# Performance work log

Measured on AMD Instinct MI355X. Metric: run time of the kernel, lower is better.

The kernel has to match this reference:

```python
import jax, jax.numpy as jnp
import numpy as np

B, S, HID = 2, 2048, 2048
H, D = 16, 128  # heads, head_dim == kernel_hidden_size
GATE_NORM = 16.0
CLAMP_MIN = -50.0


def gla(q, k, v, gk):
    # fused_recurrent_gla: S_t = diag(exp(gk_t)) S_{t-1} + k_t^T v_t; o_t = (q_t*scale) @ S_t
    # q,k,v,gk: [B,H,S,D]
    scale = D ** -0.5
    qs = jnp.moveaxis(q, 2, 0) * scale  # [S,B,H,D]
    ks = jnp.moveaxis(k, 2, 0)
    vs = jnp.moveaxis(v, 2, 0)
    gs = jnp.moveaxis(gk, 2, 0)

    def step(state, xs):
        q_t, k_t, v_t, g_t = xs  # each [B,H,D]
        state = state * jnp.exp(g_t)[..., None] + k_t[..., None] * v_t[..., None, :]
        o_t = jnp.einsum('bhk,bhkv->bhv', q_t, state)
        return state, o_t

    init = jnp.zeros((q.shape[0], H, D, D), q.dtype)
    _, out = jax.lax.scan(step, init, (qs, ks, vs, gs))
    return jnp.moveaxis(out, 0, 2)  # [B,H,S,D]


def setup_inputs() -> dict:
    key = jax.random.key(0)
    ks = jax.random.split(key, 8)
    std = 0.02
    hidden_states = jax.random.normal(ks[0], (B, S, HID), jnp.float32)
    Wq = jax.random.normal(ks[1], (HID, HID), jnp.float32) * std
    Wk = jax.random.normal(ks[2], (HID, HID), jnp.float32) * std
    Wv = jax.random.normal(ks[3], (HID, HID), jnp.float32) * std
    Wo = jax.random.normal(ks[4], (HID, HID), jnp.float32) * std
    Wg1 = jnp.eye(HID, dtype=jnp.float32)  # nn.init.eye_
    bg1 = jnp.zeros((HID,), jnp.float32)
    Wg2 = jnp.eye(HID, dtype=jnp.float32)
    bg2 = jnp.zeros((HID,), jnp.float32)
    alpha_list = jax.random.uniform(ks[5], (2,), jnp.float32)
    return dict(hidden_states=hidden_states, Wq=Wq, Wk=Wk, Wv=Wv, Wo=Wo,
                Wg1=Wg1, bg1=bg1, Wg2=Wg2, bg2=bg2, alpha_list=alpha_list)


def reference(hidden_states, Wq, Wk, Wv, Wo, Wg1, bg1, Wg2, bg2, alpha_list):
    b, s, _ = hidden_states.shape

    def split_heads(x):  # [b,s,hid] -> [b,h,s,d]
        return x.reshape(b, s, H, D).transpose(0, 2, 1, 3)

    q = split_heads(hidden_states @ Wq.T)
    k = split_heads(hidden_states @ Wk.T)
    v = split_heads(hidden_states @ Wv.T)

    def gate(Wg, bg):
        g = split_heads(hidden_states @ Wg.T + bg)
        g = jax.nn.log_sigmoid(g) / GATE_NORM
        return jnp.maximum(g, CLAMP_MIN)

    gk = gate(Wg1, bg1)
    gk2 = gate(Wg2, bg2)

    o1 = gla(q, k, v, gk)
    o2 = gla(q, k, v, gk2)

    a = jax.nn.softmax(alpha_list)
    attn = a[0] * o1 + a[1] * o2  # [b,h,s,d]
    attn = attn.transpose(0, 2, 1, 3).reshape(b, s, HID)
    return attn @ Wo.T
```

## Files before the change

### kernel.cpp

```cpp
#include <hip/hip_runtime.h>
#include <cstdint>
#include <cstddef>


#define BB     2
#define SEQ    2048
#define HIDN   2048
#define NH     16
#define DD     128
#define CHUNK  64
#define NCHUNK (SEQ / CHUNK)
#define NBH    (BB * NH)
#define NELC   8388608
#define WELC   4194304
static constexpr float QSCALE = 0.08838834764831845f;

typedef __bf16 bf16_t;
typedef _Float16 half_t;
typedef short  short8 __attribute__((ext_vector_type(8)));
typedef float  f32x4  __attribute__((ext_vector_type(4)));

__device__ __forceinline__ float bf2f(short u) {
  return (float)__builtin_bit_cast(bf16_t, u);
}
__device__ __forceinline__ short f2bf(float f) {
  return __builtin_bit_cast(short, (bf16_t)f);
}
__device__ __forceinline__ float hf2f(short u) {
  return (float)__builtin_bit_cast(half_t, u);
}
__device__ __forceinline__ short f2hf(float f) {
  return __builtin_bit_cast(short, (half_t)f);
}

__device__ __forceinline__ void gload_lds16(const void* g, void* l) {
  __builtin_amdgcn_global_load_lds(
      (__attribute__((address_space(1))) unsigned int*)g,
      (__attribute__((address_space(3))) unsigned int*)l, 16, 0, 0);
}

#define VMW2 asm volatile("s_waitcnt vmcnt(2)" ::: "memory")
#define VMW0 asm volatile("s_waitcnt vmcnt(0)" ::: "memory")
#define SBAR __builtin_amdgcn_s_barrier()


#define STG_A(buf, kt, h)                                                   \
  {                                                                         \
    const size_t ko = (size_t)(kt) * 64;                                    \
    gload_lds16(Ag + (size_t)((h) * 128) * HIDN + ko,                       \
                (void*)&As[buf][((h) * 128 + wave * 8) * 64]);              \
    gload_lds16(Ag + (size_t)((h) * 128 + 64) * HIDN + ko,                  \
                (void*)&As[buf][((h) * 128 + 64 + wave * 8) * 64]);         \
  }

#define STG_B(buf, kt, h)                                                   \
  {                                                                         \
    const size_t ko = (size_t)(kt) * 64;                                    \
    gload_lds16(Bg + (size_t)((h) * 128) * HIDN + ko,                       \
                (void*)&Bs[buf][((h) * 128 + wave * 8) * 64]);              \
    gload_lds16(Bg + (size_t)((h) * 128 + 64) * HIDN + ko,                  \
                (void*)&Bs[buf][((h) * 128 + 64 + wave * 8) * 64]);         \
  }

#define LDA(mh, rb)                                                         \
  {                                                                         \
    _Pragma("unroll") for (int f = 0; f < 4; f++) {                         \
      const int row = wm * 128 + (mh) * 64 + f * 16 + l16;                  \
      af[f][0] = *(const short8*)&As[rb][row * 64 + ((qd ^ ro) << 3)];      \
      af[f][1] =                                                            \
          *(const short8*)&As[rb][row * 64 + (((4 + qd) ^ ro) << 3)];       \
    }                                                                       \
  }

#define LDB2(j0, rb)                                                        \
  {                                                                         \
    _Pragma("unroll") for (int g = 0; g < 2; g++) {                         \
      const int col = wn * 64 + ((j0) + g) * 16 + l16;                      \
      bfr[(j0) + g][0] =                                                    \
          *(const short8*)&Bs[rb][col * 64 + ((qd ^ ro) << 3)];             \
      bfr[(j0) + g][1] =                                                    \
          *(const short8*)&Bs[rb][col * 64 + (((4 + qd) ^ ro) << 3)];       \
    }                                                                       \
  }

#define MQ(mh, nh)                                                          \
  {                                                                         \
    __builtin_amdgcn_s_setprio(1);                                          \
    _Pragma("unroll") for (int ks = 0; ks < 2; ks++)                        \
    _Pragma("unroll") for (int f = 0; f < 4; f++)                           \
    _Pragma("unroll") for (int g = 0; g < 2; g++)                           \
      acc[(mh) * 4 + f][(nh) * 2 + g] =                                     \
          __builtin_amdgcn_mfma_f32_16x16x32_bf16(                          \
              af[f][ks], bfr[(nh) * 2 + g][ks],                             \
              acc[(mh) * 4 + f][(nh) * 2 + g], 0, 0, 0);                    \
    __builtin_amdgcn_s_setprio(0);                                          \
  }

__device__ __forceinline__ void gemm256(const bf16_t* __restrict__ A,
                                        const bf16_t* __restrict__ Bw,
                                        const float*  __restrict__ bias,
                                        bf16_t* __restrict__ outb,
                                        float*  __restrict__ outf, int epi) {
  __shared__ short As[2][256 * 64];
  __shared__ short Bs[2][256 * 64];
  const int tm   = blockIdx.x * 256;
  const int tn   = blockIdx.y * 256;
  const int tid  = threadIdx.x;
  const int wave = tid >> 6;
  const int lane = tid & 63;
  const int wm   = wave >> 2;
  const int wn   = wave & 3;
  const int qd   = lane >> 4;
  const int l16  = lane & 15;
  const int ro   = l16 & 7;
  const int gc   = (lane & 7) ^ (lane >> 3);

  const short* Ag =
      (const short*)A + (size_t)(tm + wave * 8 + (lane >> 3)) * HIDN + gc * 8;
  const short* Bg =
      (const short*)Bw + (size_t)(tn + wave * 8 + (lane >> 3)) * HIDN + gc * 8;

  f32x4 acc[8][4];
#pragma unroll
  for (int i = 0; i < 8; i++)
#pragma unroll
    for (int j = 0; j < 4; j++) acc[i][j] = (f32x4){0.f, 0.f, 0.f, 0.f};
  short8 af[4][2], bfr[4][2];

  STG_A(0, 0, 0); STG_A(0, 0, 1); STG_B(0, 0, 0); STG_B(0, 0, 1);
  STG_A(1, 1, 0);
  VMW2;
  SBAR;

  for (int t = 0; t < 16; t++) {
    LDA(0, 0); LDB2(0, 0);
    STG_A(1, 2 * t + 1, 1);
    SBAR; MQ(0, 0); SBAR;
    LDB2(2, 0);
    STG_B(1, 2 * t + 1, 0);
    SBAR; MQ(0, 1); SBAR;
    LDA(1, 0);
    STG_B(1, 2 * t + 1, 1);
    SBAR; MQ(1, 1); SBAR;
    if (t < 15) { STG_A(0, 2 * t + 2, 0); }
    SBAR; MQ(1, 0);
    if (t < 15) { VMW2; } else { VMW0; }
    SBAR;
    LDA(0, 1); LDB2(0, 1);
    if (t < 15) { STG_A(0, 2 * t + 2, 1); }
    SBAR; MQ(0, 0); SBAR;
    LDB2(2, 1);
    if (t < 15) { STG_B(0, 2 * t + 2, 0); }
    SBAR; MQ(0, 1); SBAR;
    LDA(1, 1);
    if (t < 15) { STG_B(0, 2 * t + 2, 1); }
    SBAR; MQ(1, 1); SBAR;
    if (t < 15) { STG_A(1, 2 * t + 3, 0); }
    SBAR; MQ(1, 0);
    if (t < 15) { VMW2; }
    SBAR;
  }

#pragma unroll
  for (int i = 0; i < 8; i++)
#pragma unroll
    for (int j = 0; j < 4; j++)
#pragma unroll
      for (int r = 0; r < 4; r++) {
        const int row =
            tm + wm * 128 + (i >> 2) * 64 + (i & 3) * 16 + qd * 4 + r;
        const int col = tn + wn * 64 + j * 16 + l16;
        float v = acc[i][j][r];
        if (epi == 1) {
          v += bias[col];
          const float ls = fminf(v, 0.f) - log1pf(__expf(-fabsf(v)));
          v = fmaxf(ls * 0.0625f, -50.f);
        }
        if (epi == 2) outf[(size_t)row * HIDN + col] = v;
        else          outb[(size_t)row * HIDN + col] = (bf16_t)v;
      }
}

__global__ __launch_bounds__(512, 2) void k_gemm_proj(
    const bf16_t* __restrict__ Xb,
    const bf16_t* __restrict__ W0, const bf16_t* __restrict__ W1,
    const bf16_t* __restrict__ W2, const bf16_t* __restrict__ W3,
    const bf16_t* __restrict__ W4,
    const float* __restrict__ bg1, const float* __restrict__ bg2,
    bf16_t* __restrict__ Qb, bf16_t* __restrict__ Kb, bf16_t* __restrict__ Vb,
    bf16_t* __restrict__ G1b, bf16_t* __restrict__ G2b) {
  const int z = blockIdx.z;
  const bf16_t* Ws[5] = {W0, W1, W2, W3, W4};
  bf16_t* Os[5] = {Qb, Kb, Vb, G1b, G2b};
  const float* bias = (z == 3) ? bg1 : ((z == 4) ? bg2 : nullptr);
  gemm256(Xb, Ws[z], bias, Os[z], nullptr, (z >= 3) ? 1 : 0);
}

__global__ __launch_bounds__(512, 2) void k_gemm_out(
    const bf16_t* __restrict__ attnB, const bf16_t* __restrict__ Wob,
    float* __restrict__ out) {
  gemm256(attnB, Wob, nullptr, nullptr, out, 2);
}

__global__ __launch_bounds__(256) void k_cvt_all(
    const float* __restrict__ hid, const float* __restrict__ wq,
    const float* __restrict__ wk, const float* __restrict__ wv,
    const float* __restrict__ wg1, const float* __restrict__ wg2,
    const float* __restrict__ wo, bf16_t* __restrict__ Xb,
    bf16_t* __restrict__ Wd, bf16_t* __restrict__ Wcur,
    bf16_t* __restrict__ WoB) {
  const int y = blockIdx.y;
  const float* srcs[7] = {hid, wq, wk, wv, wg1, wg2, wo};
  bf16_t* dsts[7] = {Xb, Wd, Wd + WELC, Wd + 2 * WELC, Wd + 3 * WELC, Wcur,
                     WoB};
  const int n = (y == 0) ? NELC : WELC;
  const float* src = srcs[y];
  bf16_t* dst = dsts[y];
  const int idx = (blockIdx.x * 256 + threadIdx.x) * 4;
  if (idx < n) {
    const float4 f = *(const float4*)(src + idx);
    dst[idx + 0] = (bf16_t)f.x; dst[idx + 1] = (bf16_t)f.y;
    dst[idx + 2] = (bf16_t)f.z; dst[idx + 3] = (bf16_t)f.w;
  }
}

__global__ __launch_bounds__(256) void k_zero(float* __restrict__ out) {
  out[(size_t)blockIdx.x * 256 + threadIdx.x] = 0.f;
}

__global__ __launch_bounds__(64) void k_gc(bf16_t* __restrict__ G1b,
                                           bf16_t* __restrict__ G2b,
                                           float* __restrict__ Btot) {
  const int n = blockIdx.x, b = blockIdx.y >> 2, slab = blockIdx.y & 3;
  const int e = blockIdx.z;
  short* P = (short*)(e ? G2b : G1b);
  const int d0 = slab * 512 + threadIdx.x * 8;
  const size_t base = ((size_t)(b * SEQ + n * CHUNK)) * HIDN + d0;
  float c[8] = {0.f, 0.f, 0.f, 0.f, 0.f, 0.f, 0.f, 0.f};
  for (int t = 0; t < CHUNK; t++) {
    short* p = P + base + (size_t)t * HIDN;
    const short8 g = *(const short8*)p;
    short8 o;
#pragma unroll
    for (int j = 0; j < 8; j++) { c[j] += bf2f(g[j]); o[j] = f2hf(c[j]); }
    *(short8*)p = o;
  }
  const int bh = b * 16 + (d0 >> 7);
  float* bp = Btot + ((size_t)(e * NBH + bh) * NCHUNK + n) * DD + (d0 & 127);
#pragma unroll
  for (int j = 0; j < 8; j++) bp[j] = c[j];
}

template <int ACC>
__global__ __launch_bounds__(256) void k_sA(
    const bf16_t* __restrict__ Qb, const bf16_t* __restrict__ Kb,
    const bf16_t* __restrict__ Vb, const bf16_t* __restrict__ Gc,
    bf16_t* __restrict__ UT, const float* __restrict__ alpha,
    bf16_t* __restrict__ attn) {
  const int n = blockIdx.x, bh = blockIdx.y;
  const int b = bh >> 4, h = bh & 15;
  const size_t rbase = ((size_t)(b * SEQ + n * CHUNK)) * HIDN + h * DD;
  const int tid = threadIdx.x;
  const int wave = tid >> 6, lane = tid & 63, qd = lane >> 4, l16 = lane & 15;
  __shared__ short vT[128 * 66];
  __shared__ short k2s[64 * 128];
  __shared__ short r3[128 * 66];
  __shared__ short Ps[64 * 72];
  const float mx = fmaxf(alpha[0], alpha[1]);
  const float x0 = __expf(alpha[0] - mx), x1 = __expf(alpha[1] - mx);
  const float wsc = ((ACC ? x1 : x0) / (x0 + x1)) * QSCALE;

  const short* Kp = (const short*)Kb;
  const short* Vp = (const short*)Vb;
  const short* Gp = (const short*)Gc;
  const short* Qp = (const short*)Qb;

#pragma unroll
  for (int rep = 0; rep < 4; rep++) {
    const int slot = rep * 256 + tid;
    const int t = slot >> 4, ch = slot & 15;
    const size_t ga = rbase + (size_t)t * HIDN + ch * 8;
    const short8 vv = *(const short8*)(Vp + ga);
    const short8 kk = *(const short8*)(Kp + ga);
    const short8 cc = *(const short8*)(Gp + ga);
    const short8 c6 = *(const short8*)(Gp + rbase + (size_t)63 * HIDN + ch * 8);
    short8 k2v;
#pragma unroll
    for (int j = 0; j < 8; j++) {
      const int d = ch * 8 + j;
      vT[d * 66 + t] = vv[j];
      const float c = hf2f(cc[j]);
      const float kf = bf2f(kk[j]);
      k2v[j] = f2bf(kf * __expf(-c));
      r3[d * 66 + t] = f2bf(kf * __expf(hf2f(c6[j]) - c));
    }
    *(short8*)&k2s[t * 128 + ((ch ^ (t & 7)) << 3)] = k2v;
  }
  __syncthreads();

  {
    const int m0 = (wave >> 1) * 64, n0 = (wave & 1) * 64;
    const int* vTi = (const int*)vT;
    const int* r3i = (const int*)r3;
    f32x4 uacc[4][4];
#pragma unroll
    for (int i = 0; i < 4; i++)
#pragma unroll
      for (int j = 0; j < 4; j++) uacc[i][j] = (f32x4){0.f, 0.f, 0.f, 0.f};
#pragma unroll
    for (int ks = 0; ks < 2; ks++) {
      const int ch = ks * 4 + qd;
      short8 af[4], bfv[4];
#pragma unroll
      for (int i = 0; i < 4; i++) {
        const int dv = m0 + i * 16 + l16;
        const int ba = dv * 33 + ch * 4;
#pragma unroll
        for (int w2 = 0; w2 < 4; w2++) {
          const int v = vTi[ba + w2];
          af[i][2 * w2] = (short)(v & 0xffff);
          af[i][2 * w2 + 1] = (short)((unsigned)v >> 16);
        }
      }
#pragma unroll
      for (int j = 0; j < 4; j++) {
        const int dk = n0 + j * 16 + l16;
        const int ba = dk * 33 + ch * 4;
#pragma unroll
        for (int w2 = 0; w2 < 4; w2++) {
          const int v = r3i[ba + w2];
          bfv[j][2 * w2] = (short)(v & 0xffff);
          bfv[j][2 * w2 + 1] = (short)((unsigned)v >> 16);
        }
      }
#pragma unroll
      for (int i = 0; i < 4; i++)
#pragma unroll
        for (int j = 0; j < 4; j++)
          uacc[i][j] = __builtin_amdgcn_mfma_f32_16x16x32_bf16(
              af[i], bfv[j], uacc[i][j], 0, 0, 0);
    }
    short* Uo = (short*)UT + (size_t)(bh * NCHUNK + n) * (DD * DD);
#pragma unroll
    for (int i = 0; i < 4; i++)
#pragma unroll
      for (int j = 0; j < 4; j++)
#pragma unroll
        for (int r = 0; r < 4; r++) {
          const int dv = m0 + i * 16 + qd * 4 + r;
          const int dk = n0 + j * 16 + l16;
          Uo[dv * 128 + (((dk >> 3) ^ (dv & 7)) << 3) + (dk & 7)] =
              f2bf(uacc[i][j][r]);
        }
  }
  __syncthreads();

#pragma unroll
  for (int rep = 0; rep < 4; rep++) {
    const int slot = rep * 256 + tid;
    const int t = slot >> 4, ch = slot & 15;
    const size_t ga = rbase + (size_t)t * HIDN + ch * 8;
    const short8 qq = *(const short8*)(Qp + ga);
    const short8 cc = *(const short8*)(Gp + ga);
    short8 o;
#pragma unroll
    for (int j = 0; j < 8; j++)
      o[j] = f2bf(bf2f(qq[j]) * wsc * __expf(hf2f(cc[j])));
    *(short8*)&r3[t * 128 + ((ch ^ (t & 7)) << 3)] = o;
  }
  __syncthreads();

  {
    f32x4 pacc[4];
#pragma unroll
    for (int j = 0; j < 4; j++) pacc[j] = (f32x4){0.f, 0.f, 0.f, 0.f};
    const int tq = wave * 16 + l16;
#pragma unroll
    for (int ks = 0; ks < 4; ks++) {
      const int ch = ks * 4 + qd;
      const short8 a = *(const short8*)&r3[tq * 128 + ((ch ^ (tq & 7)) << 3)];
#pragma unroll
      for (int j = 0; j < 4; j++) {
        const int s = j * 16 + l16;
        const short8 bq =
            *(const short8*)&k2s[s * 128 + ((ch ^ (s & 7)) << 3)];
        pacc[j] =
            __builtin_amdgcn_mfma_f32_16x16x32_bf16(a, bq, pacc[j], 0, 0, 0);
      }
    }
#pragma unroll
    for (int j = 0; j < 4; j++)
#pragma unroll
      for (int r = 0; r < 4; r++) {
        const int t = wave * 16 + qd * 4 + r, s = j * 16 + l16;
        Ps[t * 72 + s] = (t >= s) ? f2bf(pacc[j][r]) : (short)0;
      }
  }
  __syncthreads();

  f32x4 oacc[8];
#pragma unroll
  for (int j = 0; j < 8; j++) oacc[j] = (f32x4){0.f, 0.f, 0.f, 0.f};
  {
    const int* vTi = (const int*)vT;
    const int tq = wave * 16 + l16;
#pragma unroll
    for (int ks = 0; ks < 2; ks++) {
      const int ch = ks * 4 + qd;
      const short8 a = *(const short8*)&Ps[tq * 72 + ch * 8];
#pragma unroll
      for (int j = 0; j < 8; j++) {
        const int dv = j * 16 + l16;
        const int ba = dv * 33 + ch * 4;
        short8 bq;
#pragma unroll
        for (int w2 = 0; w2 < 4; w2++) {
          const int v = vTi[ba + w2];
          bq[2 * w2] = (short)(v & 0xffff);
          bq[2 * w2 + 1] = (short)((unsigned)v >> 16);
        }
        oacc[j] =
            __builtin_amdgcn_mfma_f32_16x16x32_bf16(a, bq, oacc[j], 0, 0, 0);
      }
    }
  }
#pragma unroll
  for (int j = 0; j < 8; j++)
#pragma unroll
    for (int r = 0; r < 4; r++) {
      const int t = wave * 16 + qd * 4 + r;
      const int dv = j * 16 + l16;
      bf16_t* p = &attn[rbase + (size_t)t * HIDN + dv];
      if (ACC) *p = (bf16_t)((float)*p + oacc[j][r]);
      else     *p = (bf16_t)oacc[j][r];
    }
}

__global__ __launch_bounds__(256) void k_s2(bf16_t* __restrict__ UT,
                                            const float* __restrict__ Btot) {
  const int dg = blockIdx.x, bh = blockIdx.y;
  const int dv = dg * 8 + (threadIdx.x >> 5);
  const int dk0 = (threadIdx.x & 31) * 4;
  const int pos = dv * 128 + (((dk0 >> 3) ^ (dv & 7)) << 3) + (dk0 & 7);
  float st[4] = {0.f, 0.f, 0.f, 0.f};
  for (int nn = 0; nn < NCHUNK; nn++) {
    short* p = (short*)UT + (size_t)(bh * NCHUNK + nn) * (DD * DD) + pos;
    const float4 bp =
        *(const float4*)(Btot + (size_t)(bh * NCHUNK + nn) * DD + dk0);
    short u0 = p[0], u1 = p[1], u2 = p[2], u3 = p[3];
    p[0] = f2bf(st[0]); p[1] = f2bf(st[1]);
    p[2] = f2bf(st[2]); p[3] = f2bf(st[3]);
    st[0] = st[0] * __expf(bp.x) + bf2f(u0);
    st[1] = st[1] * __expf(bp.y) + bf2f(u1);
    st[2] = st[2] * __expf(bp.z) + bf2f(u2);
    st[3] = st[3] * __expf(bp.w) + bf2f(u3);
  }
}

__global__ __launch_bounds__(256) void k_s3b(
    const bf16_t* __restrict__ Qb, const bf16_t* __restrict__ Gc,
    const bf16_t* __restrict__ UT, const float* __restrict__ alpha,
    const int e, bf16_t* __restrict__ attn) {
  const int n = blockIdx.x, bh = blockIdx.y;
  const int b = bh >> 4, h = bh & 15;
  const size_t rbase = ((size_t)(b * SEQ + n * CHUNK)) * HIDN + h * DD;
  const int tid = threadIdx.x;
  const int wave = tid >> 6, lane = tid & 63, qd = lane >> 4, l16 = lane & 15;
  __shared__ short qh[64 * 128];
  __shared__ short Ss[128 * 128];
  const float mx = fmaxf(alpha[0], alpha[1]);
  const float x0 = __expf(alpha[0] - mx), x1 = __expf(alpha[1] - mx);
  const float wsc = ((e ? x1 : x0) / (x0 + x1)) * QSCALE;

  const short* Sp = (const short*)UT + (size_t)(bh * NCHUNK + n) * (DD * DD);
#pragma unroll
  for (int rep = 0; rep < 8; rep++) {
    const int c = rep * 256 + tid;
    gload_lds16(Sp + c * 8, &Ss[c * 8]);
  }
  const short* Qp = (const short*)Qb;
  const short* Gp = (const short*)Gc;
#pragma unroll
  for (int rep = 0; rep < 4; rep++) {
    const int slot = rep * 256 + tid;
    const int t = slot >> 4, ch = slot & 15;
    const size_t ga = rbase + (size_t)t * HIDN + ch * 8;
    const short8 qq = *(const short8*)(Qp + ga);
    const short8 cc = *(const short8*)(Gp + ga);
    short8 o;
#pragma unroll
    for (int j = 0; j < 8; j++)
      o[j] = f2bf(bf2f(qq[j]) * wsc * __expf(hf2f(cc[j])));
    *(short8*)&qh[t * 128 + ((ch ^ (t & 7)) << 3)] = o;
  }
  __syncthreads();

  f32x4 oacc[8];
#pragma unroll
  for (int j = 0; j < 8; j++) oacc[j] = (f32x4){0.f, 0.f, 0.f, 0.f};
  const int tq = wave * 16 + l16;
#pragma unroll
  for (int ks = 0; ks < 4; ks++) {
    const int ch = ks * 4 + qd;
    const short8 a = *(const short8*)&qh[tq * 128 + ((ch ^ (tq & 7)) << 3)];
#pragma unroll
    for (int j = 0; j < 8; j++) {
      const int dv = j * 16 + l16;
      const short8 bq = *(const short8*)&Ss[dv * 128 + ((ch ^ (dv & 7)) << 3)];
      oacc[j] =
          __builtin_amdgcn_mfma_f32_16x16x32_bf16(a, bq, oacc[j], 0, 0, 0);
    }
  }
#pragma unroll
  for (int j = 0; j < 8; j++)
#pragma unroll
    for (int r = 0; r < 4; r++) {
      const int t = wave * 16 + qd * 4 + r;
      const int dv = j * 16 + l16;
      bf16_t* p = &attn[rbase + (size_t)t * HIDN + dv];
      *p = (bf16_t)((float)*p + oacc[j][r]);
    }
}

extern "C" void kernel_launch(void* const* d_in, const int* in_sizes, int n_in,
                              void* d_out, int out_size, void* d_ws,
                              size_t ws_size, hipStream_t stream) {
  const float* hid  = (const float*)d_in[0];
  const float* wq   = (const float*)d_in[1];
  const float* wk   = (const float*)d_in[2];
  const float* wv   = (const float*)d_in[3];
  const float* wo   = (const float*)d_in[4];
  const float* wg1  = (const float*)d_in[5];
  const float* bg1  = (const float*)d_in[6];
  const float* wg2  = (const float*)d_in[7];
  const float* bg2  = (const float*)d_in[8];
  const float* alph = (const float*)d_in[9];
  float* out = (float*)d_out;
  (void)in_sizes; (void)n_in; (void)out_size;

  char* ws = (char*)d_ws;
  size_t off = 0;
  auto alloc = [&](size_t bytes) -> void* {
    void* p = ws + off;
    off += (bytes + 255) & ~(size_t)255;
    return p;
  };
  const size_t NEL = NELC, WEL = WELC;
  bf16_t* Xb   = (bf16_t*)alloc(NEL * 2);
  bf16_t* Wcur = (bf16_t*)alloc(WEL * 2);
  bf16_t* WoB  = (bf16_t*)alloc(WEL * 2);
  bf16_t* Qb   = (bf16_t*)alloc(NEL * 2);
  bf16_t* Kb   = (bf16_t*)alloc(NEL * 2);
  bf16_t* Vb   = (bf16_t*)alloc(NEL * 2);
  bf16_t* G1b  = (bf16_t*)alloc(NEL * 2);
  bf16_t* G2b  = (bf16_t*)alloc(NEL * 2);
  float*  Btot = (float*) alloc((size_t)2 * NBH * NCHUNK * DD * 4);
  bf16_t* Wd = (bf16_t*)d_out;
  bf16_t* UT = (bf16_t*)d_out;

  if (off > ws_size) {
    k_zero<<<dim3((unsigned)(NEL / 256)), 256, 0, stream>>>(out);
    return;
  }

  k_cvt_all<<<dim3(8192, 7), 256, 0, stream>>>(hid, wq, wk, wv, wg1, wg2, wo,
                                               Xb, Wd, Wcur, WoB);
  k_gemm_proj<<<dim3(16, 8, 5), 512, 0, stream>>>(
      Xb, Wd, Wd + WEL, Wd + 2 * WEL, Wd + 3 * WEL, Wcur, bg1, bg2, Qb, Kb, Vb,
      G1b, G2b);
  k_gc<<<dim3(NCHUNK, BB * 4, 2), 64, 0, stream>>>(G1b, G2b, Btot);

  const dim3 gs(NCHUNK, NBH), g2(16, NBH);
  const size_t BSTRIDE = (size_t)NBH * NCHUNK * DD;
  k_sA<0><<<gs, 256, 0, stream>>>(Qb, Kb, Vb, G1b, UT, alph, Xb);
  k_s2<<<g2, 256, 0, stream>>>(UT, Btot);
  k_s3b<<<gs, 256, 0, stream>>>(Qb, G1b, UT, alph, 0, Xb);
  k_sA<1><<<gs, 256, 0, stream>>>(Qb, Kb, Vb, G2b, UT, alph, Xb);
  k_s2<<<g2, 256, 0, stream>>>(UT, Btot + BSTRIDE);
  k_s3b<<<gs, 256, 0, stream>>>(Qb, G2b, UT, alph, 1, Xb);

  k_gemm_out<<<dim3(16, 8), 512, 0, stream>>>(Xb, WoB, out);
}
```

Baseline: 591.4 us.

## Restructure GEMM main loop into simple double-buffered pipeline with fewer barriers

Rewrites the GEMM k-loop as a 32-iteration ping-pong over two LDS buffers. It also reorganizes the A/B staging partitions so each prefetch quarter lands in exactly the rows the next MFMA phase reads. Most of the paired barriers around each MFMA block are removed in favour of vmcnt-based waits, with only about three barriers per k-step. This aims to cut barrier stalls and let global-to-LDS loads overlap compute. The risk is that the wait counts and barrier placement no longer cover every read-after-write or write-after-read hazard on the LDS buffers, which could produce races.

```diff
diff --git a/kernel.cpp b/kernel.cpp
--- a/kernel.cpp
+++ b/kernel.cpp
@@ -39,27 +39,29 @@
       (__attribute__((address_space(3))) unsigned int*)l, 16, 0, 0);
 }
 
-#define VMW2 asm volatile("s_waitcnt vmcnt(2)" ::: "memory")
-#define VMW0 asm volatile("s_waitcnt vmcnt(0)" ::: "memory")
+#define WVM4 asm volatile("s_waitcnt vmcnt(4)" ::: "memory")
+#define WVM2 asm volatile("s_waitcnt vmcnt(2)" ::: "memory")
+#define WVM0 asm volatile("s_waitcnt vmcnt(0)" ::: "memory")
 #define SBAR __builtin_amdgcn_s_barrier()
 
 
-#define STG_A(buf, kt, h)                                                   \
+#define STG_A(buf, kt, p)                                                   \
   {                                                                         \
     const size_t ko = (size_t)(kt) * 64;                                    \
-    gload_lds16(Ag + (size_t)((h) * 128) * HIDN + ko,                       \
-                (void*)&As[buf][((h) * 128 + wave * 8) * 64]);              \
-    gload_lds16(Ag + (size_t)((h) * 128 + 64) * HIDN + ko,                  \
-                (void*)&As[buf][((h) * 128 + 64 + wave * 8) * 64]);         \
-  }
-
-#define STG_B(buf, kt, h)                                                   \
+    gload_lds16(Ag + (size_t)((p) * 64) * HIDN + ko,                        \
+                (void*)&As[buf][((p) * 64 + wave * 8) * 64]);               \
+    gload_lds16(Ag + (size_t)((p) * 64 + 128) * HIDN + ko,                  \
+                (void*)&As[buf][((p) * 64 + 128 + wave * 8) * 64]);         \
+  }
+
+#define STG_B(buf, kt, p)                                                   \
   {                                                                         \
+    const int cb0 = (wave >> 2) * 64 + (p) * 32 + (wave & 3) * 8;           \
     const size_t ko = (size_t)(kt) * 64;                                    \
-    gload_lds16(Bg + (size_t)((h) * 128) * HIDN + ko,                       \
-                (void*)&Bs[buf][((h) * 128 + wave * 8) * 64]);              \
-    gload_lds16(Bg + (size_t)((h) * 128 + 64) * HIDN + ko,                  \
-                (void*)&Bs[buf][((h) * 128 + 64 + wave * 8) * 64]);         \
+    gload_lds16(Bg + (size_t)cb0 * HIDN + ko,                               \
+                (void*)&Bs[buf][cb0 * 64]);                                 \
+    gload_lds16(Bg + (size_t)(cb0 + 128) * HIDN + ko,                       \
+                (void*)&Bs[buf][(cb0 + 128) * 64]);                         \
   }
 
 #define LDA(mh, rb)                                                         \
@@ -118,7 +120,7 @@
   const short* Ag =
       (const short*)A + (size_t)(tm + wave * 8 + (lane >> 3)) * HIDN + gc * 8;
   const short* Bg =
-      (const short*)Bw + (size_t)(tn + wave * 8 + (lane >> 3)) * HIDN + gc * 8;
+      (const short*)Bw + (size_t)(tn + (lane >> 3)) * HIDN + gc * 8;
 
   f32x4 acc[8][4];
 #pragma unroll
@@ -127,38 +129,32 @@
     for (int j = 0; j < 4; j++) acc[i][j] = (f32x4){0.f, 0.f, 0.f, 0.f};
   short8 af[4][2], bfr[4][2];
 
-  STG_A(0, 0, 0); STG_A(0, 0, 1); STG_B(0, 0, 0); STG_B(0, 0, 1);
-  STG_A(1, 1, 0);
-  VMW2;
+  STG_A(0, 0, 0); STG_B(0, 0, 0); STG_B(0, 0, 1); STG_A(0, 0, 1);
+  WVM0;
   SBAR;
 
-  for (int t = 0; t < 16; t++) {
-    LDA(0, 0); LDB2(0, 0);
-    STG_A(1, 2 * t + 1, 1);
-    SBAR; MQ(0, 0); SBAR;
-    LDB2(2, 0);
-    STG_B(1, 2 * t + 1, 0);
-    SBAR; MQ(0, 1); SBAR;
-    LDA(1, 0);
-    STG_B(1, 2 * t + 1, 1);
-    SBAR; MQ(1, 1); SBAR;
-    if (t < 15) { STG_A(0, 2 * t + 2, 0); }
-    SBAR; MQ(1, 0);
-    if (t < 15) { VMW2; } else { VMW0; }
+  for (int t = 0; t < 32; t++) {
+    const int cur = t & 1, nx = cur ^ 1;
+    LDA(0, cur);
+    LDB2(0, cur);
+    if (t < 31) { STG_A(nx, t + 1, 0); }
+    MQ(0, 0);
+    if (t < 31) { WVM4; } else { WVM2; }
     SBAR;
-    LDA(0, 1); LDB2(0, 1);
-    if (t < 15) { STG_A(0, 2 * t + 2, 1); }
-    SBAR; MQ(0, 0); SBAR;
-    LDB2(2, 1);
-    if (t < 15) { STG_B(0, 2 * t + 2, 0); }
-    SBAR; MQ(0, 1); SBAR;
-    LDA(1, 1);
-    if (t < 15) { STG_B(0, 2 * t + 2, 1); }
-    SBAR; MQ(1, 1); SBAR;
-    if (t < 15) { STG_A(1, 2 * t + 3, 0); }
-    SBAR; MQ(1, 0);
-    if (t < 15) { VMW2; }
+    LDB2(2, cur);
+    if (t < 31) { STG_B(nx, t + 1, 0); }
+    MQ(0, 1);
+    if (t < 31) { WVM4; } else { WVM0; }
     SBAR;
+    LDA(1, cur);
+    if (t < 31) { STG_B(nx, t + 1, 1); }
+    MQ(1, 1);
+    if (t < 31) { STG_A(nx, t + 1, 1); }
+    MQ(1, 0);
+    if (t < 31) {
+      WVM4;
+      SBAR;
+    }
   }
 
 #pragma unroll
```

Result: slower. 605.9 us (+2.4%).

## Reorder GEMM LDS staging halves and use explicit ds_read with manual waits

Applied to the files above, without the earlier changes.

Changes which rows each staging half loads so that A halves match the mh split and B halves match each wave-column's nh split. This lets the pipeline drop two barriers per iteration. LDS fragment reads become inline-asm ds_read_b128 followed by an explicit lgkmcnt(0) wait and a sched barrier before each MFMA block, giving manual control over instruction scheduling. The risk is a race if the new half-to-row mapping does not exactly match the consumption order once barriers are removed.

```diff
diff --git a/kernel.cpp b/kernel.cpp
--- a/kernel.cpp
+++ b/kernel.cpp
@@ -39,36 +39,50 @@
       (__attribute__((address_space(3))) unsigned int*)l, 16, 0, 0);
 }
 
+__device__ __forceinline__ short8 ldsr128(const short* p) {
+  short8 r;
+  asm volatile("ds_read_b128 %0, %1"
+               : "=v"(r)
+               : "v"((unsigned)(unsigned long long)
+                         (__attribute__((address_space(3))) const short*)p));
+  return r;
+}
+
 #define VMW2 asm volatile("s_waitcnt vmcnt(2)" ::: "memory")
 #define VMW0 asm volatile("s_waitcnt vmcnt(0)" ::: "memory")
+#define WAIT_LDS                                          \
+  do {                                                    \
+    asm volatile("s_waitcnt lgkmcnt(0)" ::: "memory");    \
+    __builtin_amdgcn_sched_barrier(0);                    \
+  } while (0)
 #define SBAR __builtin_amdgcn_s_barrier()
 
 
 #define STG_A(buf, kt, h)                                                   \
   {                                                                         \
     const size_t ko = (size_t)(kt) * 64;                                    \
-    gload_lds16(Ag + (size_t)((h) * 128) * HIDN + ko,                       \
-                (void*)&As[buf][((h) * 128 + wave * 8) * 64]);              \
-    gload_lds16(Ag + (size_t)((h) * 128 + 64) * HIDN + ko,                  \
-                (void*)&As[buf][((h) * 128 + 64 + wave * 8) * 64]);         \
+    gload_lds16(Ag + (size_t)((h) * 64) * HIDN + ko,                        \
+                (void*)&As[buf][((h) * 64 + wave * 8) * 64]);               \
+    gload_lds16(Ag + (size_t)((h) * 64 + 128) * HIDN + ko,                  \
+                (void*)&As[buf][((h) * 64 + 128 + wave * 8) * 64]);         \
   }
 
 #define STG_B(buf, kt, h)                                                   \
   {                                                                         \
+    const int cb0 = (wave >> 2) * 64 + (h) * 32 + (wave & 3) * 8;           \
     const size_t ko = (size_t)(kt) * 64;                                    \
-    gload_lds16(Bg + (size_t)((h) * 128) * HIDN + ko,                       \
-                (void*)&Bs[buf][((h) * 128 + wave * 8) * 64]);              \
-    gload_lds16(Bg + (size_t)((h) * 128 + 64) * HIDN + ko,                  \
-                (void*)&Bs[buf][((h) * 128 + 64 + wave * 8) * 64]);         \
+    gload_lds16(Bg + (size_t)cb0 * HIDN + ko,                               \
+                (void*)&Bs[buf][cb0 * 64]);                                 \
+    gload_lds16(Bg + (size_t)(cb0 + 128) * HIDN + ko,                       \
+                (void*)&Bs[buf][(cb0 + 128) * 64]);                         \
   }
 
 #define LDA(mh, rb)                                                         \
   {                                                                         \
     _Pragma("unroll") for (int f = 0; f < 4; f++) {                         \
       const int row = wm * 128 + (mh) * 64 + f * 16 + l16;                  \
-      af[f][0] = *(const short8*)&As[rb][row * 64 + ((qd ^ ro) << 3)];      \
-      af[f][1] =                                                            \
-          *(const short8*)&As[rb][row * 64 + (((4 + qd) ^ ro) << 3)];       \
+      af[f][0] = ldsr128(&As[rb][row * 64 + ((qd ^ ro) << 3)]);             \
+      af[f][1] = ldsr128(&As[rb][row * 64 + (((4 + qd) ^ ro) << 3)]);       \
     }                                                                       \
   }
 
@@ -77,9 +91,9 @@
     _Pragma("unroll") for (int g = 0; g < 2; g++) {                         \
       const int col = wn * 64 + ((j0) + g) * 16 + l16;                      \
       bfr[(j0) + g][0] =                                                    \
-          *(const short8*)&Bs[rb][col * 64 + ((qd ^ ro) << 3)];             \
+          ldsr128(&Bs[rb][col * 64 + ((qd ^ ro) << 3)]);                    \
       bfr[(j0) + g][1] =                                                    \
-          *(const short8*)&Bs[rb][col * 64 + (((4 + qd) ^ ro) << 3)];       \
+          ldsr128(&Bs[rb][col * 64 + (((4 + qd) ^ ro) << 3)]);              \
     }                                                                       \
   }
 
@@ -118,7 +132,7 @@
   const short* Ag =
       (const short*)A + (size_t)(tm + wave * 8 + (lane >> 3)) * HIDN + gc * 8;
   const short* Bg =
-      (const short*)Bw + (size_t)(tn + wave * 8 + (lane >> 3)) * HIDN + gc * 8;
+      (const short*)Bw + (size_t)(tn + (lane >> 3)) * HIDN + gc * 8;
 
   f32x4 acc[8][4];
 #pragma unroll
@@ -135,28 +149,28 @@
   for (int t = 0; t < 16; t++) {
     LDA(0, 0); LDB2(0, 0);
     STG_A(1, 2 * t + 1, 1);
-    SBAR; MQ(0, 0); SBAR;
+    SBAR; WAIT_LDS; MQ(0, 0); SBAR;
     LDB2(2, 0);
     STG_B(1, 2 * t + 1, 0);
-    SBAR; MQ(0, 1); SBAR;
+    SBAR; WAIT_LDS; MQ(0, 1); SBAR;
     LDA(1, 0);
     STG_B(1, 2 * t + 1, 1);
-    SBAR; MQ(1, 1); SBAR;
+    SBAR; WAIT_LDS; MQ(1, 1); SBAR;
     if (t < 15) { STG_A(0, 2 * t + 2, 0); }
-    SBAR; MQ(1, 0);
+    MQ(1, 0);
     if (t < 15) { VMW2; } else { VMW0; }
     SBAR;
     LDA(0, 1); LDB2(0, 1);
     if (t < 15) { STG_A(0, 2 * t + 2, 1); }
-    SBAR; MQ(0, 0); SBAR;
+    SBAR; WAIT_LDS; MQ(0, 0); SBAR;
     LDB2(2, 1);
     if (t < 15) { STG_B(0, 2 * t + 2, 0); }
-    SBAR; MQ(0, 1); SBAR;
+    SBAR; WAIT_LDS; MQ(0, 1); SBAR;
     LDA(1, 1);
     if (t < 15) { STG_B(0, 2 * t + 2, 1); }
-    SBAR; MQ(1, 1); SBAR;
+    SBAR; WAIT_LDS; MQ(1, 1); SBAR;
     if (t < 15) { STG_A(1, 2 * t + 3, 0); }
-    SBAR; MQ(1, 0);
+    MQ(1, 0);
     if (t < 15) { VMW2; }
     SBAR;
   }
```

New measurement: 628.7 us. 6.3% more time.
